# Kernel tuning notes

Hardware: AMD Instinct MI355X
Metric: run time of the kernel (lower is better)

The kernel has to match this reference:

```python
import jax, jax.numpy as jnp
import numpy as np

B, S, D = 4, 2048, 1024
E, H, TOP_K = 8, 4096, 2


def setup_inputs() -> dict:
    key = jax.random.key(0)
    ks = jax.random.split(key, 5)
    scale = 0.02
    return {
        "x": jax.random.normal(ks[0], (B, S, D), dtype=jnp.float32),
        "Wr": jax.random.normal(ks[1], (D, E), dtype=jnp.float32) * scale,
        "br": jnp.zeros((E,), dtype=jnp.float32),
        "W1": jax.random.normal(ks[2], (E, D, H), dtype=jnp.float32) * scale,
        "b1": jnp.zeros((E, H), dtype=jnp.float32),
        "W2": jax.random.normal(ks[3], (E, H, D), dtype=jnp.float32) * scale,
        "b2": jnp.zeros((E, D), dtype=jnp.float32),
    }


def reference(x, Wr, br, W1, b1, W2, b2):
    b, s, d = x.shape
    xf = x.reshape(-1, d)                                   # [T, D]
    gate = jax.nn.softmax(xf @ Wr + br, axis=-1)            # [T, E]
    top_w, top_i = jax.lax.top_k(gate, TOP_K)               # [T, K]
    top_w = top_w / jnp.sum(top_w, axis=-1, keepdims=True)
    # combine[t, e] = sum_i top_w[t, i] * 1{top_i[t, i] == e}
    combine = jnp.sum(jax.nn.one_hot(top_i, E, dtype=xf.dtype) * top_w[..., None], axis=1)  # [T, E]
    # Dense all-expert FFN (same math as the masked per-expert loops in torch)
    h = jax.nn.gelu(jnp.einsum('td,edh->teh', xf, W1) + b1, approximate=False)  # [T, E, H]
    out = jnp.einsum('teh,ehd,te->td', h, W2, combine) + combine @ b2           # [T, D]
    return out.reshape(b, s, d)
```

## Files before the change

kernel.cpp:

```cpp
#include <hip/hip_runtime.h>
#include <cstdio>


#define T_TOK 8192
#define DIM   1024
#define NEXP  8
#define HID   4096
#define MAXR  18432

typedef float          f32x4   __attribute__((ext_vector_type(4)));
typedef short          bf16x8  __attribute__((ext_vector_type(8)));
typedef unsigned short u16x8   __attribute__((ext_vector_type(8)));
typedef unsigned short u16x4   __attribute__((ext_vector_type(4)));

static __device__ __forceinline__ unsigned short f2bf(float f) {
  unsigned int u = __builtin_bit_cast(unsigned int, f);
  u = (u + 0x7FFFu + ((u >> 16) & 1u)) >> 16;
  return (unsigned short)u;
}

static __device__ __forceinline__ void gl16(const void* g, void* l) {
  __builtin_amdgcn_global_load_lds(
      (const __attribute__((address_space(1))) unsigned int*)g,
      (__attribute__((address_space(3))) unsigned int*)l,
      16, 0, 0);
}

static __device__ __forceinline__ void transpose_body(const float* __restrict__ W,
                                                      unsigned short* __restrict__ WT,
                                                      int R, int C, int bx, int by, int e) {
  int lane = threadIdx.x & 63, w = threadIdx.x >> 6;
  int r0 = by * 64, c0 = bx * 128 + w * 32;
  int r8 = (lane & 7) * 8, cg = lane >> 3;
  const float* src = W + (size_t)e * R * C + (size_t)(r0 + r8) * C + c0 + cg * 4;
  float4 v[8];
#pragma unroll
  for (int j = 0; j < 8; ++j) v[j] = *(const float4*)(src + (size_t)j * C);
  unsigned short* dst = WT + (size_t)e * R * C + (size_t)(c0 + cg * 4) * R + r0 + r8;
#pragma unroll
  for (int s = 0; s < 4; ++s) {
    u16x8 o;
#pragma unroll
    for (int j = 0; j < 8; ++j) {
      float f = s == 0 ? v[j].x : s == 1 ? v[j].y : s == 2 ? v[j].z : v[j].w;
      o[j] = f2bf(f);
    }
    *(u16x8*)(dst + (size_t)s * R) = o;
  }
}

static __device__ __forceinline__ void router_body(int blk, const float* __restrict__ x,
                                                   const float* __restrict__ Wr,
                                                   const float* __restrict__ br,
                                                   int* __restrict__ meta,
                                                   int2* __restrict__ top_i,
                                                   float2* __restrict__ top_w) {
  int lane = threadIdx.x & 63;
  int wid  = threadIdx.x >> 6;
  int t = blk * 4 + wid;
  const float* xp = x + (size_t)t * DIM + lane * 16;
  float acc[NEXP];
#pragma unroll
  for (int e = 0; e < NEXP; ++e) acc[e] = 0.f;
#pragma unroll
  for (int j = 0; j < 16; j += 4) {
    float4 xv = *(const float4*)(xp + j);
    const float* wp = Wr + (size_t)(lane * 16 + j) * NEXP;
#pragma unroll
    for (int jj = 0; jj < 4; ++jj) {
      float xs = jj == 0 ? xv.x : jj == 1 ? xv.y : jj == 2 ? xv.z : xv.w;
      float4 w0 = *(const float4*)(wp + jj * NEXP);
      float4 w1 = *(const float4*)(wp + jj * NEXP + 4);
      acc[0] += xs * w0.x; acc[1] += xs * w0.y; acc[2] += xs * w0.z; acc[3] += xs * w0.w;
      acc[4] += xs * w1.x; acc[5] += xs * w1.y; acc[6] += xs * w1.z; acc[7] += xs * w1.w;
    }
  }
#pragma unroll
  for (int off = 32; off > 0; off >>= 1) {
#pragma unroll
    for (int e = 0; e < NEXP; ++e) acc[e] += __shfl_xor(acc[e], off);
  }
  if (lane == 0) {
    float l[NEXP];
#pragma unroll
    for (int e = 0; e < NEXP; ++e) l[e] = acc[e] + br[e];
    int e1 = 0;
#pragma unroll
    for (int e = 1; e < NEXP; ++e) if (l[e] > l[e1]) e1 = e;
    int e2 = (e1 == 0) ? 1 : 0;
#pragma unroll
    for (int e = 0; e < NEXP; ++e) if (e != e1 && l[e] > l[e2]) e2 = e;
    float g  = expf(l[e2] - l[e1]);
    float w1 = 1.f / (1.f + g);
    top_i[t] = make_int2(e1, e2);
    top_w[t] = make_float2(w1, 1.f - w1);
    atomicAdd(&meta[e1], 1);
    atomicAdd(&meta[e2], 1);
  }
}

__global__ __launch_bounds__(256) void prep_k(const float* __restrict__ W1,
                                              const float* __restrict__ W2,
                                              unsigned short* __restrict__ W1bT,
                                              unsigned short* __restrict__ W2bT,
                                              const float* __restrict__ x,
                                              const float* __restrict__ Wr,
                                              const float* __restrict__ br,
                                              int* __restrict__ meta,
                                              int2* __restrict__ top_i,
                                              float2* __restrict__ top_w,
                                              int* __restrict__ tok_of_row,
                                              float* __restrict__ wt_of_row) {
  int id = blockIdx.x;
  if (id < 4096) {
    int rem = id & 511;
    transpose_body(W1, W1bT, DIM, HID, rem & 31, rem >> 5, id >> 9);
  } else if (id < 8192) {
    int id2 = id - 4096;
    int rem = id2 & 511;
    transpose_body(W2, W2bT, HID, DIM, rem & 7, rem >> 3, id2 >> 9);
  } else if (id < 10240) {
    router_body(id - 8192, x, Wr, br, meta, top_i, top_w);
  } else {
    int i = (id - 10240) * 256 + threadIdx.x;
    if (i < MAXR) { tok_of_row[i] = 0; wt_of_row[i] = 0.f; }
  }
}

__global__ void prefix_k(int* __restrict__ meta) {
  if (threadIdx.x == 0) {
    int s = 0;
#pragma unroll
    for (int e = 0; e < NEXP; ++e) {
      meta[16 + e] = s;
      s += (meta[e] + 255) & ~255;
    }
    meta[24] = s;
    meta[25] = s;
  }
}

__global__ __launch_bounds__(256) void scatter_k(const int2* __restrict__ top_i,
                                                 const float2* __restrict__ top_w,
                                                 int* __restrict__ meta,
                                                 int* __restrict__ row_of,
                                                 int* __restrict__ tok_of_row,
                                                 float* __restrict__ wt_of_row) {
  int t = blockIdx.x * 256 + threadIdx.x;
  int2  ei = top_i[t];
  float2 w = top_w[t];
  int p = atomicAdd(&meta[8 + ei.x], 1);
  int r = meta[16 + ei.x] + p;
  tok_of_row[r] = t; wt_of_row[r] = w.x; row_of[t * 2] = r;
  p = atomicAdd(&meta[8 + ei.y], 1);
  r = meta[16 + ei.y] + p;
  tok_of_row[r] = t; wt_of_row[r] = w.y; row_of[t * 2 + 1] = r;
}

__global__ __launch_bounds__(256) void gather_k(const float* __restrict__ x,
                                                const int* __restrict__ tok_of_row,
                                                const int* __restrict__ meta,
                                                unsigned short* __restrict__ xg) {
  int r = blockIdx.x;
  if (r >= meta[25]) return;
  int t = tok_of_row[r];
  int c = threadIdx.x * 4;
  float4 v = *(const float4*)(x + (size_t)t * DIM + c);
  u16x4 o;
  o[0] = f2bf(v.x); o[1] = f2bf(v.y); o[2] = f2bf(v.z); o[3] = f2bf(v.w);
  *(u16x4*)(xg + (size_t)r * DIM + c) = o;
}


template <int KTOT, int NTOT, int EPI>
__global__ __launch_bounds__(256, 4) void gemmv12_k(const unsigned short* __restrict__ A,
                                                    const unsigned short* __restrict__ Bt,
                                                    const float* __restrict__ bias,
                                                    const int* __restrict__ meta,
                                                    const float* __restrict__ wt_of_row,
                                                    const int* __restrict__ tok_of_row,
                                                    void* __restrict__ Cout) {
  constexpr int NN  = NTOT / 128;
  constexpr int NXB = MAXR / 128;
  constexpr int NWG = NXB * NN;
  constexpr int NSR = NXB / 4;
  constexpr int NKT = KTOT / 64;
  __shared__ __align__(16) unsigned short lds[16384];

  int id = ((int)blockIdx.x & 7) * (NWG / 8) + ((int)blockIdx.x >> 3);
  int sid = id >> 4, sub = id & 15;
  int row0 = ((sid % NSR) * 4 + (sub & 3)) * 128;
  int n0   = ((sid / NSR) * 4 + (sub >> 2)) * 128;
  if (row0 >= meta[25]) return;
  int e = 0;
  while (meta[17 + e] <= row0) ++e;
  if (row0 - meta[16 + e] >= meta[e]) return;
  const unsigned short* Bp = Bt + (size_t)e * NTOT * KTOT;

  int tid = threadIdx.x;
  int lane = tid & 63, wid = tid >> 6;
  int wm = wid >> 1, wn = wid & 1;

  int s = (tid & 7) ^ ((tid >> 3) & 7);
  const unsigned short* pA = A  + (size_t)(row0 + (tid >> 3)) * KTOT + s * 8;
  const unsigned short* pB = Bp + (size_t)(n0   + (tid >> 3)) * KTOT + s * 8;

  int am = lane & 15, g = lane >> 4;
  int sw0 = ((0 * 4 + g) ^ (am & 7)) * 8;
  int sw1 = ((1 * 4 + g) ^ (am & 7)) * 8;
  int aRow = (wm * 64 + am) * 64;
  int bRow = 8192 + (wn * 64 + am) * 64;

  f32x4 acc[4][4];
#pragma unroll
  for (int i = 0; i < 4; ++i)
#pragma unroll
    for (int j = 0; j < 4; ++j) acc[i][j] = (f32x4){0.f, 0.f, 0.f, 0.f};

  for (int kt = 0; kt < NKT; ++kt) {
    __syncthreads();
#pragma unroll
    for (int i = 0; i < 4; ++i) {
      gl16(pA + (size_t)(i * 32) * KTOT + kt * 64, lds + i * 2048 + tid * 8);
      gl16(pB + (size_t)(i * 32) * KTOT + kt * 64, lds + 8192 + i * 2048 + tid * 8);
    }
    __syncthreads();
#pragma unroll
    for (int kk = 0; kk < 2; ++kk) {
      int sw = kk ? sw1 : sw0;
      bf16x8 af[4], bv[4];
#pragma unroll
      for (int i = 0; i < 4; ++i)
        af[i] = *(const bf16x8*)(lds + aRow + i * 1024 + sw);
#pragma unroll
      for (int j = 0; j < 4; ++j)
        bv[j] = *(const bf16x8*)(lds + bRow + j * 1024 + sw);
#pragma unroll
      for (int i = 0; i < 4; ++i)
#pragma unroll
        for (int j = 0; j < 4; ++j)
          acc[i][j] = __builtin_amdgcn_mfma_f32_16x16x32_bf16(af[i], bv[j], acc[i][j], 0, 0, 0);
    }
  }

  int rbase = row0 + wm * 64 + (g << 2);
  int nbase = n0 + wn * 64 + am;
  if constexpr (EPI == 0) {
    unsigned short* Hp = (unsigned short*)Cout;
    const float* bp = bias + (size_t)e * NTOT;
#pragma unroll
    for (int i = 0; i < 4; ++i)
#pragma unroll
      for (int j = 0; j < 4; ++j) {
        int n = nbase + j * 16;
        float bv = bp[n];
#pragma unroll
        for (int gg = 0; gg < 4; ++gg) {
          int m = rbase + i * 16 + gg;
          float v = acc[i][j][gg] + bv;
          v = 0.5f * v * (1.f + erff(v * 0.70710678118654752f));
          Hp[(size_t)m * NTOT + n] = f2bf(v);
        }
      }
  } else {
    float* Op = (float*)Cout;
    const float* bp = bias + (size_t)e * NTOT;
#pragma unroll
    for (int i = 0; i < 4; ++i)
#pragma unroll
      for (int gg = 0; gg < 4; ++gg) {
        int m = rbase + i * 16 + gg;
        float wt = wt_of_row[m];
        if (wt != 0.f) {
          float* orow = Op + (size_t)tok_of_row[m] * DIM;
#pragma unroll
          for (int j = 0; j < 4; ++j) {
            int n = nbase + j * 16;
            atomicAdd(orow + n, (acc[i][j][gg] + bp[n]) * wt);
          }
        }
      }
  }
}

extern "C" void kernel_launch(void* const* d_in, const int* in_sizes, int n_in,
                              void* d_out, int out_size, void* d_ws, size_t ws_size,
                              hipStream_t stream) {
  const float* x  = (const float*)d_in[0];
  const float* Wr = (const float*)d_in[1];
  const float* br = (const float*)d_in[2];
  const float* W1 = (const float*)d_in[3];
  const float* b1 = (const float*)d_in[4];
  const float* W2 = (const float*)d_in[5];
  const float* b2 = (const float*)d_in[6];
  float* out = (float*)d_out;

  char* base = (char*)d_ws;
  size_t off = 0;
  auto carve = [&](size_t bytes) -> void* {
    void* r = base + off;
    off = (off + bytes + 255) & ~(size_t)255;
    return r;
  };
  int*            meta       = (int*)carve(26 * 4);
  int2*           top_i      = (int2*)carve((size_t)T_TOK * 8);
  float2*         top_w      = (float2*)carve((size_t)T_TOK * 8);
  int*            row_of     = (int*)carve((size_t)T_TOK * 2 * 4);
  int*            tok_of_row = (int*)carve((size_t)MAXR * 4);
  float*          wt_of_row  = (float*)carve((size_t)MAXR * 4);
  unsigned short* xg         = (unsigned short*)carve((size_t)MAXR * DIM * 2);
  unsigned short* W1bT       = (unsigned short*)carve((size_t)NEXP * DIM * HID * 2);
  unsigned short* W2bT       = (unsigned short*)carve((size_t)NEXP * DIM * HID * 2);
  unsigned short* hbuf       = (unsigned short*)carve((size_t)MAXR * HID * 2);
  if (off > ws_size) {
    fprintf(stderr, "kernel_launch: ws_size too small: need %zu have %zu\n", off, ws_size);
    return;
  }

  hipMemsetAsync(meta, 0, 26 * 4, stream);
  hipMemsetAsync(out, 0, (size_t)out_size * 4, stream);
  hipLaunchKernelGGL(prep_k, dim3(10312), dim3(256), 0, stream,
                     W1, W2, W1bT, W2bT, x, Wr, br, meta, top_i, top_w,
                     tok_of_row, wt_of_row);
  hipLaunchKernelGGL(prefix_k, dim3(1), dim3(64), 0, stream, meta);
  hipLaunchKernelGGL(scatter_k, dim3(T_TOK / 256), dim3(256), 0, stream,
                     top_i, top_w, meta, row_of, tok_of_row, wt_of_row);
  hipLaunchKernelGGL(gather_k, dim3(MAXR), dim3(256), 0, stream, x, tok_of_row, meta, xg);
  hipLaunchKernelGGL((gemmv12_k<DIM, HID, 0>), dim3((MAXR / 128) * (HID / 128)), dim3(256), 0,
                     stream, xg, W1bT, b1, meta, wt_of_row, tok_of_row, (void*)hbuf);
  hipLaunchKernelGGL((gemmv12_k<HID, DIM, 1>), dim3((MAXR / 128) * (DIM / 128)), dim3(256), 0,
                     stream, hbuf, W2bT, b2, meta, wt_of_row, tok_of_row, (void*)out);
}
```

Before: 814.7 us.

## Store bf16 weights in k8-interleaved layout instead of a full transpose

```diff
diff --git a/kernel.cpp b/kernel.cpp
--- a/kernel.cpp
+++ b/kernel.cpp
@@ -26,38 +26,53 @@
       16, 0, 0);
 }
 
-static __device__ __forceinline__ void transpose_body(const float* __restrict__ W,
-                                                      unsigned short* __restrict__ WT,
-                                                      int R, int C, int bx, int by, int e) {
-  int lane = threadIdx.x & 63, w = threadIdx.x >> 6;
-  int r0 = by * 64, c0 = bx * 128 + w * 32;
-  int r8 = (lane & 7) * 8, cg = lane >> 3;
-  const float* src = W + (size_t)e * R * C + (size_t)(r0 + r8) * C + c0 + cg * 4;
-  float4 v[8];
-#pragma unroll
-  for (int j = 0; j < 8; ++j) v[j] = *(const float4*)(src + (size_t)j * C);
-  unsigned short* dst = WT + (size_t)e * R * C + (size_t)(c0 + cg * 4) * R + r0 + r8;
-#pragma unroll
-  for (int s = 0; s < 4; ++s) {
-    u16x8 o;
-#pragma unroll
-    for (int j = 0; j < 8; ++j) {
-      float f = s == 0 ? v[j].x : s == 1 ? v[j].y : s == 2 ? v[j].z : v[j].w;
-      o[j] = f2bf(f);
-    }
-    *(u16x8*)(dst + (size_t)s * R) = o;
-  }
-}
-
-static __device__ __forceinline__ void router_body(int blk, const float* __restrict__ x,
-                                                   const float* __restrict__ Wr,
-                                                   const float* __restrict__ br,
-                                                   int* __restrict__ meta,
-                                                   int2* __restrict__ top_i,
-                                                   float2* __restrict__ top_w) {
+__global__ __launch_bounds__(256) void tile_k(const float* __restrict__ W1,
+                                              const float* __restrict__ W2,
+                                              unsigned short* __restrict__ T1,
+                                              unsigned short* __restrict__ T2) {
+  __shared__ unsigned short sl[8 * 1028];
+  int id = blockIdx.x;
+  const float* W; unsigned short* T; int K, N, blk;
+  if (id < 1024) { W = W1; T = T1; K = DIM; N = HID; blk = id; }
+  else           { W = W2; T = T2; K = HID; N = DIM; blk = id - 1024; }
+  int kpb = K / 8;
+  int e = blk / kpb, k8 = blk % kpb;
+  const float* src = W + (size_t)e * K * N + (size_t)k8 * 8 * N;
+  unsigned short* dst = T + (size_t)e * K * N + (size_t)k8 * 8 * N;
+  int t = threadIdx.x;
+  int kr = t >> 5, f4 = (t & 31) * 4;
+  int nchunk = N / 1024;
+  for (int c = 0; c < nchunk; ++c) {
+    if (c) __syncthreads();
+#pragma unroll
+    for (int u = 0; u < 8; ++u) {
+      int col = f4 + u * 128;
+      float4 v = *(const float4*)(src + (size_t)kr * N + c * 1024 + col);
+      u16x4 o;
+      o[0] = f2bf(v.x); o[1] = f2bf(v.y); o[2] = f2bf(v.z); o[3] = f2bf(v.w);
+      *(u16x4*)(sl + kr * 1028 + col) = o;
+    }
+    __syncthreads();
+#pragma unroll
+    for (int j = 0; j < 4; ++j) {
+      int n = t * 4 + j;
+      u16x8 o;
+#pragma unroll
+      for (int k = 0; k < 8; ++k) o[k] = sl[k * 1028 + n];
+      *(u16x8*)(dst + ((size_t)c * 1024 + n) * 8) = o;
+    }
+  }
+}
+
+__global__ __launch_bounds__(256) void router_k(const float* __restrict__ x,
+                                                const float* __restrict__ Wr,
+                                                const float* __restrict__ br,
+                                                int* __restrict__ meta,
+                                                int2* __restrict__ top_i,
+                                                float2* __restrict__ top_w) {
   int lane = threadIdx.x & 63;
   int wid  = threadIdx.x >> 6;
-  int t = blk * 4 + wid;
+  int t = blockIdx.x * 4 + wid;
   const float* xp = x + (size_t)t * DIM + lane * 16;
   float acc[NEXP];
 #pragma unroll
@@ -99,32 +114,10 @@
   }
 }
 
-__global__ __launch_bounds__(256) void prep_k(const float* __restrict__ W1,
-                                              const float* __restrict__ W2,
-                                              unsigned short* __restrict__ W1bT,
-                                              unsigned short* __restrict__ W2bT,
-                                              const float* __restrict__ x,
-                                              const float* __restrict__ Wr,
-                                              const float* __restrict__ br,
-                                              int* __restrict__ meta,
-                                              int2* __restrict__ top_i,
-                                              float2* __restrict__ top_w,
-                                              int* __restrict__ tok_of_row,
+__global__ __launch_bounds__(256) void fill_k(int* __restrict__ tok_of_row,
                                               float* __restrict__ wt_of_row) {
-  int id = blockIdx.x;
-  if (id < 4096) {
-    int rem = id & 511;
-    transpose_body(W1, W1bT, DIM, HID, rem & 31, rem >> 5, id >> 9);
-  } else if (id < 8192) {
-    int id2 = id - 4096;
-    int rem = id2 & 511;
-    transpose_body(W2, W2bT, HID, DIM, rem & 7, rem >> 3, id2 >> 9);
-  } else if (id < 10240) {
-    router_body(id - 8192, x, Wr, br, meta, top_i, top_w);
-  } else {
-    int i = (id - 10240) * 256 + threadIdx.x;
-    if (i < MAXR) { tok_of_row[i] = 0; wt_of_row[i] = 0.f; }
-  }
+  int i = blockIdx.x * 256 + threadIdx.x;
+  if (i < MAXR) { tok_of_row[i] = 0; wt_of_row[i] = 0.f; }
 }
 
 __global__ void prefix_k(int* __restrict__ meta) {
@@ -173,8 +166,8 @@
 
 
 template <int KTOT, int NTOT, int EPI>
-__global__ __launch_bounds__(256, 4) void gemmv12_k(const unsigned short* __restrict__ A,
-                                                    const unsigned short* __restrict__ Bt,
+__global__ __launch_bounds__(256, 4) void gemmv15_k(const unsigned short* __restrict__ A,
+                                                    const unsigned short* __restrict__ Wt,
                                                     const float* __restrict__ bias,
                                                     const int* __restrict__ meta,
                                                     const float* __restrict__ wt_of_row,
@@ -195,15 +188,15 @@
   int e = 0;
   while (meta[17 + e] <= row0) ++e;
   if (row0 - meta[16 + e] >= meta[e]) return;
-  const unsigned short* Bp = Bt + (size_t)e * NTOT * KTOT;
+  const unsigned short* Wp = Wt + (size_t)e * (size_t)KTOT * NTOT;
 
   int tid = threadIdx.x;
   int lane = tid & 63, wid = tid >> 6;
   int wm = wid >> 1, wn = wid & 1;
 
   int s = (tid & 7) ^ ((tid >> 3) & 7);
-  const unsigned short* pA = A  + (size_t)(row0 + (tid >> 3)) * KTOT + s * 8;
-  const unsigned short* pB = Bp + (size_t)(n0   + (tid >> 3)) * KTOT + s * 8;
+  const unsigned short* pA = A + (size_t)(row0 + (tid >> 3)) * KTOT + s * 8;
+  const unsigned short* pB = Wp + ((size_t)s * NTOT + n0 + (tid >> 3)) * 8;
 
   int am = lane & 15, g = lane >> 4;
   int sw0 = ((0 * 4 + g) ^ (am & 7)) * 8;
@@ -222,7 +215,8 @@
 #pragma unroll
     for (int i = 0; i < 4; ++i) {
       gl16(pA + (size_t)(i * 32) * KTOT + kt * 64, lds + i * 2048 + tid * 8);
-      gl16(pB + (size_t)(i * 32) * KTOT + kt * 64, lds + 8192 + i * 2048 + tid * 8);
+      gl16(pB + (size_t)(i * 32) * 8 + (size_t)kt * 64 * NTOT,
+           lds + 8192 + i * 2048 + tid * 8);
     }
     __syncthreads();
 #pragma unroll
@@ -309,8 +303,8 @@
   int*            tok_of_row = (int*)carve((size_t)MAXR * 4);
   float*          wt_of_row  = (float*)carve((size_t)MAXR * 4);
   unsigned short* xg         = (unsigned short*)carve((size_t)MAXR * DIM * 2);
-  unsigned short* W1bT       = (unsigned short*)carve((size_t)NEXP * DIM * HID * 2);
-  unsigned short* W2bT       = (unsigned short*)carve((size_t)NEXP * DIM * HID * 2);
+  unsigned short* W1t        = (unsigned short*)carve((size_t)NEXP * DIM * HID * 2);
+  unsigned short* W2t        = (unsigned short*)carve((size_t)NEXP * DIM * HID * 2);
   unsigned short* hbuf       = (unsigned short*)carve((size_t)MAXR * HID * 2);
   if (off > ws_size) {
     fprintf(stderr, "kernel_launch: ws_size too small: need %zu have %zu\n", off, ws_size);
@@ -319,15 +313,17 @@
 
   hipMemsetAsync(meta, 0, 26 * 4, stream);
   hipMemsetAsync(out, 0, (size_t)out_size * 4, stream);
-  hipLaunchKernelGGL(prep_k, dim3(10312), dim3(256), 0, stream,
-                     W1, W2, W1bT, W2bT, x, Wr, br, meta, top_i, top_w,
+  hipLaunchKernelGGL(tile_k, dim3(1024 + 4096), dim3(256), 0, stream, W1, W2, W1t, W2t);
+  hipLaunchKernelGGL(router_k, dim3(T_TOK / 4), dim3(256), 0, stream,
+                     x, Wr, br, meta, top_i, top_w);
+  hipLaunchKernelGGL(fill_k, dim3(MAXR / 256), dim3(256), 0, stream,
                      tok_of_row, wt_of_row);
   hipLaunchKernelGGL(prefix_k, dim3(1), dim3(64), 0, stream, meta);
   hipLaunchKernelGGL(scatter_k, dim3(T_TOK / 256), dim3(256), 0, stream,
                      top_i, top_w, meta, row_of, tok_of_row, wt_of_row);
   hipLaunchKernelGGL(gather_k, dim3(MAXR), dim3(256), 0, stream, x, tok_of_row, meta, xg);
-  hipLaunchKernelGGL((gemmv12_k<DIM, HID, 0>), dim3((MAXR / 128) * (HID / 128)), dim3(256), 0,
-                     stream, xg, W1bT, b1, meta, wt_of_row, tok_of_row, (void*)hbuf);
-  hipLaunchKernelGGL((gemmv12_k<HID, DIM, 1>), dim3((MAXR / 128) * (DIM / 128)), dim3(256), 0,
-                     stream, hbuf, W2bT, b2, meta, wt_of_row, tok_of_row, (void*)out);
-}
+  hipLaunchKernelGGL((gemmv15_k<DIM, HID, 0>), dim3((MAXR / 128) * (HID / 128)), dim3(256), 0,
+                     stream, xg, W1t, b1, meta, wt_of_row, tok_of_row, (void*)hbuf);
+  hipLaunchKernelGGL((gemmv15_k<HID, DIM, 1>), dim3((MAXR / 128) * (DIM / 128)), dim3(256), 0,
+                     stream, hbuf, W2t, b2, meta, wt_of_row, tok_of_row, (void*)out);
+}
```

New measurement: 905.9 us. +11.2%, slower.
